# Optimization experiments

Hardware: AMD Instinct MI355X
Metric: run time of the kernel (lower is better)

Reference implementation:

```python
import jax, jax.numpy as jnp
import numpy as np

B, S, T, E, H, V = 32, 64, 64, 512, 512, 32000  # batch, src len, tgt len, embed, hidden(per dir), vocab


def _lstm_scan(xs, Wih, Whh, bih, bhh, h0, c0):
    # xs: [S, B, E]; PyTorch gate order i, f, g, o
    def step(carry, x):
        h, c = carry
        g = x @ Wih.T + bih + h @ Whh.T + bhh
        i, f, gg, o = jnp.split(g, 4, axis=-1)
        c = jax.nn.sigmoid(f) * c + jax.nn.sigmoid(i) * jnp.tanh(gg)
        h = jax.nn.sigmoid(o) * jnp.tanh(c)
        return (h, c), h
    (hT, cT), hs = jax.lax.scan(step, (h0, c0), xs)
    return hs, hT, cT


def setup_inputs() -> dict:
    key = jax.random.key(0)
    ks = jax.random.split(key, 20)
    p = lambda k, shape, s=0.05: (jax.random.normal(k, shape, jnp.float32) * s)
    inp = {
        "input_chunk": jax.random.randint(ks[0], (B, S), 0, V),
        "target_chunk": jax.random.randint(ks[1], (B, T), 0, V),
        "enc_emb": jax.random.uniform(ks[2], (V, E), jnp.float32, -0.1, 0.1),
        "dec_emb": jax.random.uniform(ks[3], (V, E), jnp.float32, -0.1, 0.1),
        # encoder bidirectional LSTM (1 layer)
        "Wih_f": p(ks[4], (4 * H, E)), "Whh_f": p(ks[5], (4 * H, H)),
        "bih_f": p(ks[6], (4 * H,)), "bhh_f": p(ks[7], (4 * H,)),
        "Wih_b": p(ks[8], (4 * H, E)), "Whh_b": p(ks[9], (4 * H, H)),
        "bih_b": p(ks[10], (4 * H,)), "bhh_b": p(ks[11], (4 * H,)),
        # decoder LSTMCell: input 2H+E, hidden 2H
        "Wih_d": p(ks[12], (8 * H, 2 * H + E)), "Whh_d": p(ks[13], (8 * H, 2 * H)),
        "bih_d": p(ks[14], (8 * H,)), "bhh_d": p(ks[15], (8 * H,)),
        # attention projection 2H -> 2H
        "Wa": p(ks[16], (2 * H, 2 * H)), "ba": p(ks[17], (2 * H,)),
        # output projection 2H -> V (bias initialized to 0 in the module)
        "Wout": p(ks[18], (V, 2 * H)), "bout": jnp.zeros((V,), jnp.float32),
    }
    return inp


def reference(input_chunk, target_chunk, enc_emb, dec_emb,
              Wih_f, Whh_f, bih_f, bhh_f, Wih_b, Whh_b, bih_b, bhh_b,
              Wih_d, Whh_d, bih_d, bhh_d, Wa, ba, Wout, bout):
    # ---- Encoder: bidirectional LSTM ----
    x = enc_emb[input_chunk]                 # [B, S, E]
    xs = jnp.transpose(x, (1, 0, 2))         # [S, B, E]
    h0 = jnp.zeros((B, H), x.dtype)
    c0 = jnp.zeros((B, H), x.dtype)
    hs_f, hT_f, cT_f = _lstm_scan(xs, Wih_f, Whh_f, bih_f, bhh_f, h0, c0)
    hs_b, hT_b, cT_b = _lstm_scan(xs[::-1], Wih_b, Whh_b, bih_b, bhh_b, h0, c0)
    hs_b = hs_b[::-1]
    all_hidden = jnp.concatenate([hs_f, hs_b], axis=-1)          # [S, B, 2H]
    all_hidden = jnp.transpose(all_hidden, (1, 0, 2))            # [B, S, 2H]
    dec_h = jnp.concatenate([hT_f, hT_b], axis=-1)               # [B, 2H]
    dec_c = jnp.concatenate([cT_f, cT_b], axis=-1)               # [B, 2H]

    # ---- Decoder: attention + LSTMCell loop (teacher forcing = 1.0, no dropout) ----
    A = all_hidden @ Wa.T + ba               # W_attention(all_hidden), constant across steps
    tgt_emb = dec_emb[target_chunk]          # [B, T, E]
    # feed at t=0 is zeros; afterwards the t-th target embedding
    feeds = jnp.concatenate([jnp.zeros((B, 1, E), tgt_emb.dtype), tgt_emb[:, :-1]], axis=1)
    feeds = jnp.transpose(feeds, (1, 0, 2))  # [T, B, E]

    def dstep(carry, feed):
        h, c = carry
        scores = jnp.einsum('bsd,bd->bs', A, h)                  # [B, S]
        attn = jax.nn.softmax(scores, axis=1)
        ctx = jnp.einsum('bs,bsd->bd', attn, all_hidden)         # [B, 2H]
        inp = jnp.concatenate([ctx, feed], axis=1)               # [B, 2H+E]
        g = inp @ Wih_d.T + bih_d + h @ Whh_d.T + bhh_d
        i, f, gg, o = jnp.split(g, 4, axis=-1)
        c = jax.nn.sigmoid(f) * c + jax.nn.sigmoid(i) * jnp.tanh(gg)
        h = jax.nn.sigmoid(o) * jnp.tanh(c)
        logits = h @ Wout.T + bout                               # [B, V]
        return (h, c), logits

    _, logits = jax.lax.scan(dstep, (dec_h, dec_c), feeds)       # [T, B, V]
    logits = jnp.transpose(logits, (1, 0, 2))                    # [B, T, V]
    outputs = jnp.argmax(logits, axis=-1)                        # [B, T]
    return logits, outputs
```

## Files before the change

kernel.cpp:

```cpp
#include <hip/hip_runtime.h>
#include <hip/hip_bf16.h>

#define BB 32
#define SS 64
#define TT 64
#define EE 512
#define HH 512
#define VV 32000

#define O_C0    0u
#define O_C1    32768u
#define O_HD    65536u
#define O_CD    98304u
#define O_PENC  131072u
#define O_PDEC  655360u
#define O_CTX   1179648u
#define O_ALLH  1212416u
#define O_AATT  3309568u
#define O_HDEC  5406720u
#define O_PACK  7503872u
#define O_DA1   7507968u
#define O_DA2   7540736u
#define O_W1    7573504u
#define WS_NEED 95830016ull

#define S_GXF   0u
#define S_GXB   4194304u
#define S_GFEED 8388608u
#define U_BASE  17000000u
#define U_WIHF  10485760u
#define U_WIHB  11534336u
#define U_WFEED 12582912u
#define U_TOTAL 14680064u

typedef float f32x4 __attribute__((ext_vector_type(4)));
typedef _Float16 f16x8 __attribute__((ext_vector_type(8)));
typedef _Float16 f16x4 __attribute__((ext_vector_type(4)));

__device__ __forceinline__ float sigm_(float x){ return 1.0f/(1.0f + expf(-x)); }

__device__ __forceinline__ unsigned int fkey_(float f){
  unsigned int u = __float_as_uint(f);
  return (u & 0x80000000u) ? ~u : (u | 0x80000000u);
}

__device__ __forceinline__ int swz_(int row, int kb){
  return (row*64 + kb) ^ ((row & 7) << 4);
}

__global__ __launch_bounds__(256) void k_init(float* __restrict__ ws){
  int i = blockIdx.x*256 + threadIdx.x;
  if (i < 65536) ws[i] = 0.0f;
  if (i < 2048) ((unsigned long long*)(ws + O_PACK))[i] = 0ull;
}

__global__ __launch_bounds__(256) void k_cvtW(
    const float* __restrict__ Whh_f, const float* __restrict__ Whh_b,
    const float* __restrict__ Wih_d, const float* __restrict__ Whh_d,
    const float* __restrict__ Wih_f, const float* __restrict__ Wih_b,
    _Float16* __restrict__ dst)
{
  int g = blockIdx.x*256 + threadIdx.x;
  unsigned idx = (unsigned)g*4u;
  if (idx >= U_TOTAL) return;
  f32x4 v;
  if (idx < 1048576u){
    v = *(const f32x4*)(Whh_f + idx);
  } else if (idx < 2097152u){
    v = *(const f32x4*)(Whh_b + (idx - 1048576u));
  } else if (idx < U_WIHF){
    unsigned j = idx - 2097152u;
    unsigned row = j >> 11, col = j & 2047u;
    const float* src = (col < 1024u) ? (Wih_d + (size_t)row*1536 + col)
                                     : (Whh_d + (size_t)row*1024 + (col - 1024u));
    v = *(const f32x4*)src;
  } else if (idx < U_WIHB){
    v = *(const f32x4*)(Wih_f + (idx - U_WIHF));
  } else if (idx < U_WFEED){
    v = *(const f32x4*)(Wih_b + (idx - U_WIHB));
  } else {
    unsigned j = idx - U_WFEED;
    unsigned row = j >> 9, col = j & 511u;
    v = *(const f32x4*)(Wih_d + (size_t)row*1536 + 1024 + col);
  }
  f16x4 h;
  #pragma unroll
  for (int c = 0; c < 4; ++c) h[c] = (_Float16)v[c];
  *(f16x4*)(dst + idx) = h;
}

__global__ __launch_bounds__(256) void k_cvtWout(
    const float* __restrict__ Wout, _Float16* __restrict__ W1)
{
  size_t i = ((size_t)blockIdx.x*256 + threadIdx.x)*8;
  f32x4 x0 = *(const f32x4*)(Wout + i);
  f32x4 x1 = *(const f32x4*)(Wout + i + 4);
  f16x4 h0, h1;
  #pragma unroll
  for (int c = 0; c < 4; ++c){ h0[c] = (_Float16)x0[c]; h1[c] = (_Float16)x1[c]; }
  *(f16x4*)(W1 + i)   = h0;
  *(f16x4*)(W1 + i+4) = h1;
}

template<int MODE>
__global__ __launch_bounds__(256) void k_gemm(
    const float* __restrict__ A, int lda,
    const int* __restrict__ chunk,
    const float* __restrict__ W, int ldW,
    const float* __restrict__ bias0, const float* __restrict__ bias1,
    float* __restrict__ C, int ldC, int K)
{
  __shared__ float As[16*68];
  __shared__ float Bs[16*68];
  int tid = threadIdx.x;
  int n0 = blockIdx.x*64, m0 = blockIdx.y*64;
  int tx = tid & 15, ty = tid >> 4;
  int lrow = tid >> 2, kq = tid & 3;

  const float* arp;
  if (MODE == 0) {
    arp = A + (size_t)(m0 + lrow)*lda;
  } else if (MODE == 1) {
    int m = m0 + lrow; int s = m >> 5, b = m & 31;
    arp = A + (size_t)chunk[b*SS + s]*EE;
  } else {
    int m = m0 + lrow; int t = m >> 5, b = m & 31;
    arp = (t == 0) ? nullptr : A + (size_t)chunk[b*TT + (t-1)]*EE;
  }
  const float* wrp = W + (size_t)(n0 + lrow)*ldW;

  float acc[4][4] = {};
  for (int k0 = 0; k0 < K; k0 += 16){
    float4 va = make_float4(0.f,0.f,0.f,0.f);
    if (MODE == 0) va = *(const float4*)&arp[k0 + kq*4];
    else if (arp)  va = *(const float4*)&arp[k0 + kq*4];
    float4 vw = *(const float4*)&wrp[k0 + kq*4];
    As[(kq*4+0)*68 + lrow] = va.x;
    As[(kq*4+1)*68 + lrow] = va.y;
    As[(kq*4+2)*68 + lrow] = va.z;
    As[(kq*4+3)*68 + lrow] = va.w;
    Bs[(kq*4+0)*68 + lrow] = vw.x;
    Bs[(kq*4+1)*68 + lrow] = vw.y;
    Bs[(kq*4+2)*68 + lrow] = vw.z;
    Bs[(kq*4+3)*68 + lrow] = vw.w;
    __syncthreads();
    #pragma unroll
    for (int kk = 0; kk < 16; ++kk){
      float4 a4 = *(const float4*)&As[kk*68 + ty*4];
      float4 b4 = *(const float4*)&Bs[kk*68 + tx*4];
      float av[4] = {a4.x,a4.y,a4.z,a4.w};
      float bv[4] = {b4.x,b4.y,b4.z,b4.w};
      #pragma unroll
      for (int i=0;i<4;++i)
        #pragma unroll
        for (int j=0;j<4;++j)
          acc[i][j] = fmaf(av[i], bv[j], acc[i][j]);
    }
    __syncthreads();
  }
  float bv[4];
  #pragma unroll
  for (int j = 0; j < 4; ++j){
    int n = n0 + tx*4 + j;
    float bb = 0.f;
    if (bias0) bb += bias0[n];
    if (bias1) bb += bias1[n];
    bv[j] = bb;
  }
  #pragma unroll
  for (int i = 0; i < 4; ++i){
    int m = m0 + ty*4 + i;
    float4 v = make_float4(acc[i][0]+bv[0], acc[i][1]+bv[1], acc[i][2]+bv[2], acc[i][3]+bv[3]);
    *(float4*)&C[(size_t)m*ldC + n0 + tx*4] = v;
  }
}

template<int MODE>
__global__ __launch_bounds__(256) void k_proj(
    const float* __restrict__ emb, const int* __restrict__ chunk,
    const _Float16* __restrict__ Wh,
    const float* __restrict__ bias0, const float* __restrict__ bias1,
    float* __restrict__ C, int ldC)
{
  __shared__ char lds[49152];
  int tid = threadIdx.x;
  int n0 = blockIdx.x*128, m0 = blockIdx.y*128;
  int lane = tid & 63, wave = tid >> 6;
  int wm = wave >> 1, wn = wave & 1;
  int lr = lane & 15, lg = lane >> 4;

  int s0 = tid*2, s1 = tid*2 + 1;
  int ar0 = s0 >> 2, as0 = s0 & 3;
  int ar1 = s1 >> 2, as1 = s1 & 3;

  const float* arp0; const float* arp1;
  {
    int m = m0 + ar0;
    if (MODE == 1){ int s = m >> 5, b = m & 31; arp0 = emb + (size_t)chunk[b*SS + s]*EE + as0*8; }
    else { int tt = m >> 5, b = m & 31; arp0 = tt ? (emb + (size_t)chunk[b*TT + (tt-1)]*EE + as0*8) : nullptr; }
    m = m0 + ar1;
    if (MODE == 1){ int s = m >> 5, b = m & 31; arp1 = emb + (size_t)chunk[b*SS + s]*EE + as1*8; }
    else { int tt = m >> 5, b = m & 31; arp1 = tt ? (emb + (size_t)chunk[b*TT + (tt-1)]*EE + as1*8) : nullptr; }
  }
  const _Float16* wp0 = Wh + (size_t)(n0 + ar0)*512u + as0*8;
  const _Float16* wp1 = Wh + (size_t)(n0 + ar1)*512u + as1*8;

  f32x4 accH[4][4], accM[4][4];
  #pragma unroll
  for (int i = 0; i < 4; ++i)
    #pragma unroll
    for (int j = 0; j < 4; ++j){
      f32x4 z; z[0]=z[1]=z[2]=z[3]=0.f;
      accH[i][j] = z; accM[i][j] = z;
    }

  f32x4 zz; zz[0]=zz[1]=zz[2]=zz[3]=0.f;
  f32x4 a0a, a0b, a1a, a1b;
  uint4 rw0, rw1;
  a0a = arp0 ? *(const f32x4*)(arp0)     : zz;
  a0b = arp0 ? *(const f32x4*)(arp0 + 4) : zz;
  a1a = arp1 ? *(const f32x4*)(arp1)     : zz;
  a1b = arp1 ? *(const f32x4*)(arp1 + 4) : zz;
  rw0 = *(const uint4*)wp0;
  rw1 = *(const uint4*)wp1;

  for (int kt = 0; kt < 16; ++kt){
    char* base = lds + (kt & 1)*24576;
    char* A1t = base, *A2t = base + 8192, *Wt = base + 16384;
    f16x8 h0, l0, h1, l1;
    #pragma unroll
    for (int c = 0; c < 4; ++c){
      float x = a0a[c]; _Float16 hh = (_Float16)x;
      h0[c] = hh; l0[c] = (_Float16)((x - (float)hh)*2048.0f);
      x = a0b[c]; hh = (_Float16)x;
      h0[4+c] = hh; l0[4+c] = (_Float16)((x - (float)hh)*2048.0f);
      x = a1a[c]; hh = (_Float16)x;
      h1[c] = hh; l1[c] = (_Float16)((x - (float)hh)*2048.0f);
      x = a1b[c]; hh = (_Float16)x;
      h1[4+c] = hh; l1[4+c] = (_Float16)((x - (float)hh)*2048.0f);
    }
    *(f16x8*)(A1t + swz_(ar0, as0*16)) = h0;
    *(f16x8*)(A2t + swz_(ar0, as0*16)) = l0;
    *(f16x8*)(A1t + swz_(ar1, as1*16)) = h1;
    *(f16x8*)(A2t + swz_(ar1, as1*16)) = l1;
    *(uint4*)(Wt + swz_(ar0, as0*16)) = rw0;
    *(uint4*)(Wt + swz_(ar1, as1*16)) = rw1;
    __syncthreads();
    if (kt < 15){
      int ko = (kt+1)*32;
      a0a = arp0 ? *(const f32x4*)(arp0 + ko)     : zz;
      a0b = arp0 ? *(const f32x4*)(arp0 + ko + 4) : zz;
      a1a = arp1 ? *(const f32x4*)(arp1 + ko)     : zz;
      a1b = arp1 ? *(const f32x4*)(arp1 + ko + 4) : zz;
      rw0 = *(const uint4*)(wp0 + ko);
      rw1 = *(const uint4*)(wp1 + ko);
    }
    f16x8 wf[4];
    #pragma unroll
    for (int nf = 0; nf < 4; ++nf)
      wf[nf] = *(const f16x8*)(Wt + swz_(wn*64 + nf*16 + lr, lg*16));
    #pragma unroll
    for (int mf = 0; mf < 4; ++mf){
      int ad = swz_(wm*64 + mf*16 + lr, lg*16);
      f16x8 a1f = *(const f16x8*)(A1t + ad);
      f16x8 a2f = *(const f16x8*)(A2t + ad);
      #pragma unroll
      for (int nf = 0; nf < 4; ++nf){
        accH[mf][nf] = __builtin_amdgcn_mfma_f32_16x16x32_f16(a1f, wf[nf], accH[mf][nf], 0, 0, 0);
        accM[mf][nf] = __builtin_amdgcn_mfma_f32_16x16x32_f16(a2f, wf[nf], accM[mf][nf], 0, 0, 0);
      }
    }
    __syncthreads();
  }

  const float rs = 1.0f/2048.0f;
  float bb[4];
  #pragma unroll
  for (int nf = 0; nf < 4; ++nf){
    int n = n0 + wn*64 + nf*16 + lr;
    bb[nf] = bias0[n] + bias1[n];
  }
  #pragma unroll
  for (int mf = 0; mf < 4; ++mf){
    #pragma unroll
    for (int r = 0; r < 4; ++r){
      int m = m0 + wm*64 + mf*16 + lg*4 + r;
      #pragma unroll
      for (int nf = 0; nf < 4; ++nf){
        int n = n0 + wn*64 + nf*16 + lr;
        C[(size_t)m*ldC + n] = accH[mf][nf][r] + accM[mf][nf][r]*rs + bb[nf];
      }
    }
  }
}

__global__ __launch_bounds__(256) void k_enc_step(
    const _Float16* __restrict__ wenc,
    float* __restrict__ ws, const float* __restrict__ oscr, int t)
{
  __shared__ float hl[128*36];
  __shared__ float Wt[32*132];
  int sub = blockIdx.x, kp = blockIdx.y, dir = blockIdx.z;
  int tid = threadIdx.x;
  int s = dir ? (63 - t) : t;
  int p = t & 1;
  const float* gx  = oscr + (dir ? S_GXB : S_GXF);
  const float* prd = ws + (p ? O_PDEC : O_PENC) + dir*262144u;
  const float* cin = ws + O_C0 + p*32768u + dir*16384u;
  float* cout = ws + O_C0 + (p^1)*32768u + dir*16384u;

  {
    int ug = tid & 31, bg = tid >> 5;
    int ul0 = ug*4;
    int u0 = kp*128 + ul0;
    #pragma unroll
    for (int j = 0; j < 4; ++j){
      int b = bg*4 + j;
      size_t gbase = (size_t)(s*32 + b)*2048u;
      f32x4 g0 = *(const f32x4*)&gx[gbase + u0];
      f32x4 g1 = *(const f32x4*)&gx[gbase + 512 + u0];
      f32x4 g2 = *(const f32x4*)&gx[gbase + 1024 + u0];
      f32x4 g3 = *(const f32x4*)&gx[gbase + 1536 + u0];
      if (t > 0){
        #pragma unroll
        for (int kq = 0; kq < 4; ++kq){
          const float* pp = prd + kq*65536u + (size_t)b*2048u;
          g0 += *(const f32x4*)&pp[u0];
          g1 += *(const f32x4*)&pp[512 + u0];
          g2 += *(const f32x4*)&pp[1024 + u0];
          g3 += *(const f32x4*)&pp[1536 + u0];
        }
      }
      f32x4 c = *(const f32x4*)&cin[b*512 + u0];
      f32x4 cn, hn;
      #pragma unroll
      for (int e = 0; e < 4; ++e){
        float cc = sigm_(g1[e])*c[e] + sigm_(g0[e])*tanhf(g2[e]);
        float hh = sigm_(g3[e])*tanhf(cc);
        cn[e] = cc; hn[e] = hh;
        hl[(ul0+e)*36 + b] = hh;
      }
      if (sub == 0){
        *(f32x4*)&cout[b*512 + u0] = cn;
        *(f32x4*)&ws[O_ALLH + (size_t)(b*64 + s)*1024u + dir*512 + u0] = hn;
      }
    }
  }
  __syncthreads();
  if (t == 63) return;

  const _Float16* W = wenc + dir*1048576u;
  float* P = ws + (p ? O_PENC : O_PDEC) + dir*262144u + kp*65536u;
  int rg2 = tid & 31, bg2 = tid >> 5;
  int wrow = tid & 127, whalf = tid >> 7;
  float acc[4][4] = {};
  for (int kt = 0; kt < 4; ++kt){
    #pragma unroll
    for (int i = 0; i < 4; ++i){
      int chunk = whalf*4 + i;
      int grow = sub*128 + wrow;
      f16x4 v = *(const f16x4*)&W[(size_t)grow*512 + kp*128 + kt*32 + chunk*4];
      Wt[(chunk*4+0)*132 + wrow] = (float)v[0];
      Wt[(chunk*4+1)*132 + wrow] = (float)v[1];
      Wt[(chunk*4+2)*132 + wrow] = (float)v[2];
      Wt[(chunk*4+3)*132 + wrow] = (float)v[3];
    }
    __syncthreads();
    #pragma unroll 8
    for (int kk = 0; kk < 32; ++kk){
      f32x4 wv = *(const f32x4*)&Wt[kk*132 + rg2*4];
      f32x4 hv = *(const f32x4*)&hl[(kt*32+kk)*36 + bg2*4];
      #pragma unroll
      for (int i = 0; i < 4; ++i)
        #pragma unroll
        for (int j = 0; j < 4; ++j)
          acc[i][j] = fmaf(wv[i], hv[j], acc[i][j]);
    }
    __syncthreads();
  }
  #pragma unroll
  for (int j = 0; j < 4; ++j){
    int b = bg2*4 + j;
    f32x4 v; v[0]=acc[0][j]; v[1]=acc[1][j]; v[2]=acc[2][j]; v[3]=acc[3][j];
    *(f32x4*)&P[(size_t)b*2048u + sub*128 + rg2*4] = v;
  }
}

__global__ __launch_bounds__(256) void k_concat(float* __restrict__ ws){
  int i = blockIdx.x*256 + threadIdx.x;
  int which = i >> 15;
  int idx = i & 32767;
  int b = idx >> 10, u = idx & 1023;
  int dir = (u >= 512);
  int uu = u & 511;
  float v;
  if (which == 0){
    int s = dir ? 0 : 63;
    v = ws[O_ALLH + (size_t)(b*64 + s)*1024u + u];
  } else {
    v = ws[O_C0 + dir*16384u + b*512 + uu];
  }
  ws[(which ? O_CD : O_HD) + b*1024 + u] = v;
}

__global__ __launch_bounds__(256) void k_dec_gemm(
    const _Float16* __restrict__ wdec, float* __restrict__ ws)
{
  __shared__ char lds[16384];
  int nb = blockIdx.x, kp = blockIdx.y;
  int tid = threadIdx.x;
  int lane = tid & 63, w = tid >> 6;
  int lr = lane & 15, lg = lane >> 4;
  const _Float16* A1g = (const _Float16*)(ws + O_DA1);
  const _Float16* A2g = (const _Float16*)(ws + O_DA2);

  int aslot = tid & 127;
  int isA2  = tid >> 7;
  int arow = aslot >> 2, aseg = aslot & 3;
  int wrow = tid >> 2, wseg = tid & 3;
  const _Float16* asrc = (isA2 ? A2g : A1g) + (size_t)arow*2048u + kp*512 + aseg*8;
  const _Float16* wsrc = wdec + (size_t)(nb*64 + wrow)*2048u + kp*512 + wseg*8;

  f32x4 accH[2], accM[2];
  #pragma unroll
  for (int i = 0; i < 2; ++i){ f32x4 z; z[0]=z[1]=z[2]=z[3]=0.f; accH[i]=z; accM[i]=z; }

  uint4 rA = *(const uint4*)(asrc);
  uint4 rW = *(const uint4*)(wsrc);

  for (int kt = 0; kt < 16; ++kt){
    int cur = kt & 1;
    char* base = lds + cur*8192;
    *(uint4*)(base + (isA2 ? 2048 : 0) + swz_(arow, aseg*16)) = rA;
    *(uint4*)(base + 4096 + swz_(wrow, wseg*16)) = rW;
    __syncthreads();
    if (kt < 15){
      rA = *(const uint4*)(asrc + (kt+1)*32);
      rW = *(const uint4*)(wsrc + (kt+1)*32);
    }
    char* A1t = base, *A2t = base + 2048, *Wt = base + 4096;
    f16x8 wf = *(const f16x8*)(Wt + swz_(w*16 + lr, lg*16));
    #pragma unroll
    for (int mf = 0; mf < 2; ++mf){
      f16x8 a1 = *(const f16x8*)(A1t + swz_(mf*16 + lr, lg*16));
      f16x8 a2 = *(const f16x8*)(A2t + swz_(mf*16 + lr, lg*16));
      accH[mf] = __builtin_amdgcn_mfma_f32_16x16x32_f16(a1, wf, accH[mf], 0, 0, 0);
      accM[mf] = __builtin_amdgcn_mfma_f32_16x16x32_f16(a2, wf, accM[mf], 0, 0, 0);
    }
    __syncthreads();
  }
  const float rs = 1.0f/2048.0f;
  float* P = ws + O_PDEC + (size_t)kp*131072u;
  #pragma unroll
  for (int mf = 0; mf < 2; ++mf)
    #pragma unroll
    for (int r = 0; r < 4; ++r){
      int b = mf*16 + lg*4 + r;
      int n = nb*64 + w*16 + lr;
      P[(size_t)b*4096u + n] = accH[mf][r] + accM[mf][r]*rs;
    }
}

__global__ __launch_bounds__(256) void k_attn(float* __restrict__ ws,
                                              const float* __restrict__ oscr, int t){
  __shared__ float hlq[1024];
  __shared__ float part[64][5];
  __shared__ float sc[64];
  __shared__ float atn[64];
  __shared__ float dsh;
  int b = blockIdx.x, tid = threadIdx.x;
  float* hd = ws + O_HD;
  float* cd = ws + O_CD;
  _Float16* DA1 = (_Float16*)(ws + O_DA1);
  _Float16* DA2 = (_Float16*)(ws + O_DA2);
  if (t > 0){
    const float* gfd = oscr + S_GFEED + (size_t)((t-1)*32 + b)*4096u;
    const float* pd = ws + O_PDEC;
    for (int u = tid; u < 1024; u += 256){
      float g0 = gfd[u], g1 = gfd[1024+u], g2 = gfd[2048+u], g3 = gfd[3072+u];
      #pragma unroll
      for (int kp = 0; kp < 4; ++kp){
        const float* p = pd + (size_t)kp*131072u + (size_t)b*4096u;
        g0 += p[u]; g1 += p[1024+u]; g2 += p[2048+u]; g3 += p[3072+u];
      }
      float c = cd[b*1024 + u];
      c = sigm_(g1)*c + sigm_(g0)*tanhf(g2);
      float h = sigm_(g3)*tanhf(c);
      cd[b*1024+u] = c; hd[b*1024+u] = h; hlq[u] = h;
      ws[O_HDEC + (size_t)(b*64 + (t-1))*1024u + u] = h;
      _Float16 hi = (_Float16)h;
      DA1[(size_t)b*2048u + 1024 + u] = hi;
      DA2[(size_t)b*2048u + 1024 + u] = (_Float16)((h - (float)hi)*2048.0f);
    }
  } else {
    for (int u = tid; u < 1024; u += 256){
      float h = hd[b*1024 + u];
      hlq[u] = h;
      _Float16 hi = (_Float16)h;
      DA1[(size_t)b*2048u + 1024 + u] = hi;
      DA2[(size_t)b*2048u + 1024 + u] = (_Float16)((h - (float)hi)*2048.0f);
    }
  }
  __syncthreads();
  {
    int s = tid >> 2, p = tid & 3;
    const float* Ar = ws + O_AATT + (size_t)(b*64 + s)*1024u + p*256;
    const float* hp = &hlq[p*256];
    float sum = 0.f;
    #pragma unroll 8
    for (int k4 = 0; k4 < 64; ++k4){
      float4 a = *(const float4*)&Ar[k4*4];
      float4 h4 = *(const float4*)&hp[k4*4];
      sum = fmaf(a.x,h4.x, fmaf(a.y,h4.y, fmaf(a.z,h4.z, fmaf(a.w,h4.w, sum))));
    }
    part[s][p] = sum;
  }
  __syncthreads();
  if (tid < 64) sc[tid] = part[tid][0] + part[tid][1] + part[tid][2] + part[tid][3];
  __syncthreads();
  if (tid < 64){
    float m = sc[0];
    #pragma unroll
    for (int i = 1; i < 64; ++i) m = fmaxf(m, sc[i]);
    atn[tid] = expf(sc[tid] - m);
  }
  __syncthreads();
  if (tid == 0){
    float d = 0.f;
    #pragma unroll
    for (int i = 0; i < 64; ++i) d += atn[i];
    dsh = 1.0f/d;
  }
  __syncthreads();
  {
    float rd = dsh;
    float ax=0.f, ay=0.f, az=0.f, aw=0.f;
    const float* ah = ws + O_ALLH + (size_t)(b*64)*1024u + tid*4;
    for (int s2 = 0; s2 < 64; ++s2){
      float a = atn[s2];
      float4 v = *(const float4*)&ah[(size_t)s2*1024u];
      ax = fmaf(a, v.x, ax); ay = fmaf(a, v.y, ay);
      az = fmaf(a, v.z, az); aw = fmaf(a, v.w, aw);
    }
    float o[4] = {ax*rd, ay*rd, az*rd, aw*rd};
    #pragma unroll
    for (int j = 0; j < 4; ++j){
      int u = tid*4 + j;
      _Float16 hi = (_Float16)o[j];
      DA1[(size_t)b*2048u + u] = hi;
      DA2[(size_t)b*2048u + u] = (_Float16)((o[j] - (float)hi)*2048.0f);
    }
  }
}

__global__ __launch_bounds__(256) void k_fin(float* __restrict__ ws,
                                             const float* __restrict__ oscr){
  int bid = blockIdx.x, tid = threadIdx.x;
  if ((bid & 3) == 3){
    int b = bid >> 2;
    const float* gfd = oscr + S_GFEED + (size_t)(63*32 + b)*4096u;
    const float* pd = ws + O_PDEC;
    for (int q = 0; q < 4; ++q){
      int u = q*256 + tid;
      float g0 = gfd[u], g1 = gfd[1024+u], g2 = gfd[2048+u], g3 = gfd[3072+u];
      #pragma unroll
      for (int kp = 0; kp < 4; ++kp){
        const float* p = pd + (size_t)kp*131072u + (size_t)b*4096u;
        g0 += p[u]; g1 += p[1024+u]; g2 += p[2048+u]; g3 += p[3072+u];
      }
      float c = ws[O_CD + b*1024 + u];
      c = sigm_(g1)*c + sigm_(g0)*tanhf(g2);
      float h = sigm_(g3)*tanhf(c);
      ws[O_HDEC + (size_t)(b*64 + 63)*1024u + u] = h;
    }
  }
  __syncthreads();
  const float* src = ws + O_HDEC;
  _Float16* A1 = (_Float16*)(ws + O_ALLH);
  _Float16* A2 = (_Float16*)(ws + O_AATT);
  for (int rep = 0; rep < 8; ++rep){
    int i = bid*16384 + (rep*256 + tid)*8;
    f32x4 x0 = *(const f32x4*)&src[i];
    f32x4 x1 = *(const f32x4*)&src[i+4];
    f16x4 h0, h1, l0, l1;
    #pragma unroll
    for (int c = 0; c < 4; ++c){
      _Float16 a = (_Float16)x0[c];
      h0[c] = a; l0[c] = (_Float16)((x0[c] - (float)a)*2048.0f);
      _Float16 bq = (_Float16)x1[c];
      h1[c] = bq; l1[c] = (_Float16)((x1[c] - (float)bq)*2048.0f);
    }
    *(f16x4*)&A1[i]   = h0;
    *(f16x4*)&A1[i+4] = h1;
    *(f16x4*)&A2[i]   = l0;
    *(f16x4*)&A2[i+4] = l1;
  }
}

__global__ __launch_bounds__(256) void k_logits(
    const _Float16* __restrict__ A1, const _Float16* __restrict__ A2,
    const _Float16* __restrict__ W1, const float* __restrict__ bout,
    float* __restrict__ out, unsigned long long* __restrict__ pk)
{
  __shared__ char lds[49152];
  int tid = threadIdx.x;
  int n0 = blockIdx.y*128, m0 = blockIdx.x*128;
  int lane = tid & 63, wave = tid >> 6;
  int wm = wave >> 1, wn = wave & 1;
  int lr = lane & 15, lg = lane >> 4;

  int s0 = tid*2, s1 = tid*2 + 1;
  int ar0 = s0 >> 2, as0 = s0 & 3;
  int ar1 = s1 >> 2, as1 = s1 & 3;
  const _Float16* a1p0 = A1 + (size_t)(m0 + ar0)*1024u + as0*8;
  const _Float16* a1p1 = A1 + (size_t)(m0 + ar1)*1024u + as1*8;
  const _Float16* a2p0 = A2 + (size_t)(m0 + ar0)*1024u + as0*8;
  const _Float16* a2p1 = A2 + (size_t)(m0 + ar1)*1024u + as1*8;
  const _Float16* wp0  = W1 + (size_t)(n0 + ar0)*1024u + as0*8;
  const _Float16* wp1  = W1 + (size_t)(n0 + ar1)*1024u + as1*8;

  f32x4 accH[4][4], accM[4][4];
  #pragma unroll
  for (int i = 0; i < 4; ++i)
    #pragma unroll
    for (int j = 0; j < 4; ++j){
      f32x4 z; z[0]=z[1]=z[2]=z[3]=0.f;
      accH[i][j] = z; accM[i][j] = z;
    }

  uint4 r10, r11, r20, r21, rw0, rw1;
  r10 = *(const uint4*)a1p0; r11 = *(const uint4*)a1p1;
  r20 = *(const uint4*)a2p0; r21 = *(const uint4*)a2p1;
  rw0 = *(const uint4*)wp0;  rw1 = *(const uint4*)wp1;

  for (int kt = 0; kt < 32; ++kt){
    int cur = kt & 1;
    char* base = lds + cur*24576;
    char* A1t = base, *A2t = base + 8192, *Wt = base + 16384;
    *(uint4*)(A1t + swz_(ar0, as0*16)) = r10;
    *(uint4*)(A1t + swz_(ar1, as1*16)) = r11;
    *(uint4*)(A2t + swz_(ar0, as0*16)) = r20;
    *(uint4*)(A2t + swz_(ar1, as1*16)) = r21;
    *(uint4*)(Wt  + swz_(ar0, as0*16)) = rw0;
    *(uint4*)(Wt  + swz_(ar1, as1*16)) = rw1;
    __syncthreads();
    if (kt < 31){
      int ko = (kt+1)*32;
      r10 = *(const uint4*)(a1p0 + ko); r11 = *(const uint4*)(a1p1 + ko);
      r20 = *(const uint4*)(a2p0 + ko); r21 = *(const uint4*)(a2p1 + ko);
      rw0 = *(const uint4*)(wp0 + ko);  rw1 = *(const uint4*)(wp1 + ko);
    }
    f16x8 wf[4];
    #pragma unroll
    for (int nf = 0; nf < 4; ++nf)
      wf[nf] = *(const f16x8*)(Wt + swz_(wn*64 + nf*16 + lr, lg*16));
    #pragma unroll
    for (int mf = 0; mf < 4; ++mf){
      int ad = swz_(wm*64 + mf*16 + lr, lg*16);
      f16x8 a1f = *(const f16x8*)(A1t + ad);
      f16x8 a2f = *(const f16x8*)(A2t + ad);
      #pragma unroll
      for (int nf = 0; nf < 4; ++nf){
        accH[mf][nf] = __builtin_amdgcn_mfma_f32_16x16x32_f16(a1f, wf[nf], accH[mf][nf], 0, 0, 0);
        accM[mf][nf] = __builtin_amdgcn_mfma_f32_16x16x32_f16(a2f, wf[nf], accM[mf][nf], 0, 0, 0);
      }
    }
    __syncthreads();
  }

  const float rs = 1.0f/2048.0f;
  float bb[4];
  #pragma unroll
  for (int nf = 0; nf < 4; ++nf) bb[nf] = bout[n0 + wn*64 + nf*16 + lr];
  #pragma unroll
  for (int mf = 0; mf < 4; ++mf){
    #pragma unroll
    for (int r = 0; r < 4; ++r){
      int m = m0 + wm*64 + mf*16 + lg*4 + r;
      unsigned long long bk = 0ull;
      #pragma unroll
      for (int nf = 0; nf < 4; ++nf){
        int n = n0 + wn*64 + nf*16 + lr;
        float val = accH[mf][nf][r] + accM[mf][nf][r]*rs + bb[nf];
        __builtin_nontemporal_store(val, &out[(size_t)m*VV + n]);
        unsigned long long p = ((unsigned long long)fkey_(val) << 32) | (unsigned int)(~(unsigned int)n);
        if (p > bk) bk = p;
      }
      #pragma unroll
      for (int off = 1; off < 16; off <<= 1){
        unsigned long long o = __shfl_xor(bk, off, 64);
        if (o > bk) bk = o;
      }
      if (lr == 0) atomicMax(&pk[m], bk);
    }
  }
}

__global__ __launch_bounds__(512) void k_logits_fb(
    const _Float16* __restrict__ A1, const _Float16* __restrict__ A2,
    const float* __restrict__ Wout, const float* __restrict__ bout,
    float* __restrict__ out, unsigned long long* __restrict__ pk)
{
  __shared__ char lds[49152];
  char* A1t = lds;
  char* A2t = lds + 8192;
  char* W1t = lds + 16384;
  char* W2t = lds + 32768;
  int tid = threadIdx.x;
  int n0 = blockIdx.x*256;
  int lane = tid & 63, wave = tid >> 6;
  int wm = wave >> 2, wn = wave & 3;
  int lr = lane & 15, lg = lane >> 4;

  int arow = tid >> 2, aseg = tid & 3;
  int wrow = tid >> 1, wseg = tid & 1;
  const float* wp = Wout + (size_t)(n0 + wrow)*1024u + wseg*16;

  float bb[4];
  #pragma unroll
  for (int nf = 0; nf < 4; ++nf) bb[nf] = bout[n0 + wn*64 + nf*16 + lr];
  const float rs = 1.0f/2048.0f;

  for (int mi = 0; mi < 4; ++mi){
    int m0 = (blockIdx.y*4 + mi)*128;
    const _Float16* a1p = A1 + (size_t)(m0 + arow)*1024u + aseg*8;
    const _Float16* a2p = A2 + (size_t)(m0 + arow)*1024u + aseg*8;

    f32x4 accH[4][4], accM[4][4];
    #pragma unroll
    for (int i = 0; i < 4; ++i)
      #pragma unroll
      for (int j = 0; j < 4; ++j){
        f32x4 z; z[0]=z[1]=z[2]=z[3]=0.f;
        accH[i][j] = z; accM[i][j] = z;
      }

    for (int k0 = 0; k0 < 1024; k0 += 32){
      uint4 av1 = *(const uint4*)(a1p + k0);
      uint4 av2 = *(const uint4*)(a2p + k0);
      f32x4 wv[4];
      #pragma unroll
      for (int i = 0; i < 4; ++i) wv[i] = *(const f32x4*)(wp + k0 + i*4);
      __syncthreads();
      *(uint4*)(A1t + swz_(arow, aseg*16)) = av1;
      *(uint4*)(A2t + swz_(arow, aseg*16)) = av2;
      f16x8 hi[2], lo[2];
      #pragma unroll
      for (int i = 0; i < 2; ++i)
        #pragma unroll
        for (int c = 0; c < 8; ++c){
          float x = wv[i*2 + (c>>2)][c&3];
          _Float16 h = (_Float16)x;
          hi[i][c] = h;
          lo[i][c] = (_Float16)((x - (float)h)*2048.0f);
        }
      *(f16x8*)(W1t + swz_(wrow, wseg*32 +  0)) = hi[0];
      *(f16x8*)(W1t + swz_(wrow, wseg*32 + 16)) = hi[1];
      *(f16x8*)(W2t + swz_(wrow, wseg*32 +  0)) = lo[0];
      *(f16x8*)(W2t + swz_(wrow, wseg*32 + 16)) = lo[1];
      __syncthreads();
      f16x8 w1f[4], w2f[4];
      #pragma unroll
      for (int nf = 0; nf < 4; ++nf){
        int ad = swz_(wn*64 + nf*16 + lr, lg*16);
        w1f[nf] = *(const f16x8*)(W1t + ad);
        w2f[nf] = *(const f16x8*)(W2t + ad);
      }
      #pragma unroll
      for (int mf = 0; mf < 4; ++mf){
        int ad = swz_(wm*64 + mf*16 + lr, lg*16);
        f16x8 a1f = *(const f16x8*)(A1t + ad);
        f16x8 a2f = *(const f16x8*)(A2t + ad);
        #pragma unroll
        for (int nf = 0; nf < 4; ++nf){
          accH[mf][nf] = __builtin_amdgcn_mfma_f32_16x16x32_f16(a1f, w1f[nf], accH[mf][nf], 0, 0, 0);
          accM[mf][nf] = __builtin_amdgcn_mfma_f32_16x16x32_f16(a1f, w2f[nf], accM[mf][nf], 0, 0, 0);
          accM[mf][nf] = __builtin_amdgcn_mfma_f32_16x16x32_f16(a2f, w1f[nf], accM[mf][nf], 0, 0, 0);
        }
      }
    }

    #pragma unroll
    for (int mf = 0; mf < 4; ++mf){
      #pragma unroll
      for (int r = 0; r < 4; ++r){
        int m = m0 + wm*64 + mf*16 + lg*4 + r;
        unsigned long long bk = 0ull;
        #pragma unroll
        for (int nf = 0; nf < 4; ++nf){
          int n = n0 + wn*64 + nf*16 + lr;
          float val = accH[mf][nf][r] + accM[mf][nf][r]*rs + bb[nf];
          __builtin_nontemporal_store(val, &out[(size_t)m*VV + n]);
          unsigned long long p = ((unsigned long long)fkey_(val) << 32) | (unsigned int)(~(unsigned int)n);
          if (p > bk) bk = p;
        }
        #pragma unroll
        for (int off = 1; off < 16; off <<= 1){
          unsigned long long o = __shfl_xor(bk, off, 64);
          if (o > bk) bk = o;
        }
        if (lr == 0) atomicMax(&pk[m], bk);
      }
    }
  }
}

__global__ __launch_bounds__(256) void k_argmax(
    const unsigned long long* __restrict__ pk, float* __restrict__ out)
{
  int i = blockIdx.x*256 + threadIdx.x;
  if (i < 2048){
    unsigned int low = (unsigned int)(pk[i] & 0xFFFFFFFFull);
    unsigned int col = ~low;
    out[(size_t)BB*TT*VV + i] = (float)col;
  }
}

extern "C" void kernel_launch(void* const* d_in, const int* in_sizes, int n_in,
                              void* d_out, int out_size, void* d_ws, size_t ws_size,
                              hipStream_t stream)
{
  const int*   input_chunk  = (const int*)d_in[0];
  const int*   target_chunk = (const int*)d_in[1];
  const float* enc_emb = (const float*)d_in[2];
  const float* dec_emb = (const float*)d_in[3];
  const float* Wih_f = (const float*)d_in[4];
  const float* Whh_f = (const float*)d_in[5];
  const float* bih_f = (const float*)d_in[6];
  const float* bhh_f = (const float*)d_in[7];
  const float* Wih_b = (const float*)d_in[8];
  const float* Whh_b = (const float*)d_in[9];
  const float* bih_b = (const float*)d_in[10];
  const float* bhh_b = (const float*)d_in[11];
  const float* Wih_d = (const float*)d_in[12];
  const float* Whh_d = (const float*)d_in[13];
  const float* bih_d = (const float*)d_in[14];
  const float* bhh_d = (const float*)d_in[15];
  const float* Wa   = (const float*)d_in[16];
  const float* ba   = (const float*)d_in[17];
  const float* Wout = (const float*)d_in[18];
  const float* bout = (const float*)d_in[19];
  float* ws = (float*)d_ws;
  float* out = (float*)d_out;
  float* oscr = (float*)d_out;
  _Float16* wf16 = (_Float16*)(oscr + U_BASE);
  bool bigws = (ws_size >= WS_NEED);

  k_init<<<256, 256, 0, stream>>>(ws);
  k_cvtW<<<14336, 256, 0, stream>>>(Whh_f, Whh_b, Wih_d, Whh_d, Wih_f, Wih_b, wf16);
  if (bigws)
    k_cvtWout<<<16000, 256, 0, stream>>>(Wout, (_Float16*)(ws + O_W1));

  k_proj<1><<<dim3(16,16), 256, 0, stream>>>(enc_emb, input_chunk, wf16 + U_WIHF, bih_f, bhh_f, oscr + S_GXF, 2048);
  k_proj<1><<<dim3(16,16), 256, 0, stream>>>(enc_emb, input_chunk, wf16 + U_WIHB, bih_b, bhh_b, oscr + S_GXB, 2048);
  k_proj<2><<<dim3(32,16), 256, 0, stream>>>(dec_emb, target_chunk, wf16 + U_WFEED, bih_d, bhh_d, oscr + S_GFEED, 4096);

  for (int t = 0; t < 64; ++t){
    k_enc_step<<<dim3(16,4,2), 256, 0, stream>>>(wf16, ws, oscr, t);
  }

  k_concat<<<256, 256, 0, stream>>>(ws);
  k_gemm<0><<<dim3(16,32), 256, 0, stream>>>(ws + O_ALLH, 1024, nullptr, Wa, 1024, ba, nullptr, ws + O_AATT, 1024, 1024);

  const _Float16* wdec = wf16 + 2097152u;
  for (int t = 0; t < 64; ++t){
    k_attn<<<32, 256, 0, stream>>>(ws, oscr, t);
    k_dec_gemm<<<dim3(64,4), 256, 0, stream>>>(wdec, ws);
  }
  k_fin<<<128, 256, 0, stream>>>(ws, oscr);

  if (bigws){
    k_logits<<<dim3(16,250), 256, 0, stream>>>(
        (const _Float16*)(ws + O_ALLH), (const _Float16*)(ws + O_AATT),
        (const _Float16*)(ws + O_W1), bout, out, (unsigned long long*)(ws + O_PACK));
  } else {
    k_logits_fb<<<dim3(125,4), 512, 0, stream>>>(
        (const _Float16*)(ws + O_ALLH), (const _Float16*)(ws + O_AATT),
        Wout, bout, out, (unsigned long long*)(ws + O_PACK));
  }
  k_argmax<<<8, 256, 0, stream>>>((const unsigned long long*)(ws + O_PACK), out);
}
```

Measured before the change: 3.315 ms.

## Route attention projection through MFMA proj kernel and stream logits A-operand from registers

Replaces the scalar FP32 tiled GEMM for the attention projection (all_hidden @ Wa) with the existing split-fp16 MFMA projection kernel, generalized to a runtime K and a plain row-major mode. Wa is converted to fp16 along with the other weights. Separately, the logits kernel now loads the A1/A2 fragments directly from global memory into registers, prefetched one k-step ahead, and stages only the weight tile in LDS. This cuts LDS use and traffic, at the cost of uncoalesced per-lane global loads and more live registers.

```diff
diff --git a/kernel.cpp b/kernel.cpp
--- a/kernel.cpp
+++ b/kernel.cpp
@@ -10,11 +10,10 @@
 
 #define O_C0    0u
 #define O_C1    32768u
+#define O_PENC  131072u
+#define O_PDEC  655360u
 #define O_HD    65536u
 #define O_CD    98304u
-#define O_PENC  131072u
-#define O_PDEC  655360u
-#define O_CTX   1179648u
 #define O_ALLH  1212416u
 #define O_AATT  3309568u
 #define O_HDEC  5406720u
@@ -31,7 +30,8 @@
 #define U_WIHF  10485760u
 #define U_WIHB  11534336u
 #define U_WFEED 12582912u
-#define U_TOTAL 14680064u
+#define U_WA    14680064u
+#define U_TOTAL 15728640u
 
 typedef float f32x4 __attribute__((ext_vector_type(4)));
 typedef _Float16 f16x8 __attribute__((ext_vector_type(8)));
@@ -58,6 +58,7 @@
     const float* __restrict__ Whh_f, const float* __restrict__ Whh_b,
     const float* __restrict__ Wih_d, const float* __restrict__ Whh_d,
     const float* __restrict__ Wih_f, const float* __restrict__ Wih_b,
+    const float* __restrict__ Wa,
     _Float16* __restrict__ dst)
 {
   int g = blockIdx.x*256 + threadIdx.x;
@@ -78,10 +79,12 @@
     v = *(const f32x4*)(Wih_f + (idx - U_WIHF));
   } else if (idx < U_WFEED){
     v = *(const f32x4*)(Wih_b + (idx - U_WIHB));
-  } else {
+  } else if (idx < U_WA){
     unsigned j = idx - U_WFEED;
     unsigned row = j >> 9, col = j & 511u;
     v = *(const f32x4*)(Wih_d + (size_t)row*1536 + 1024 + col);
+  } else {
+    v = *(const f32x4*)(Wa + (idx - U_WA));
   }
   f16x4 h;
   #pragma unroll
@@ -103,81 +106,8 @@
 }
 
 template<int MODE>
-__global__ __launch_bounds__(256) void k_gemm(
-    const float* __restrict__ A, int lda,
-    const int* __restrict__ chunk,
-    const float* __restrict__ W, int ldW,
-    const float* __restrict__ bias0, const float* __restrict__ bias1,
-    float* __restrict__ C, int ldC, int K)
-{
-  __shared__ float As[16*68];
-  __shared__ float Bs[16*68];
-  int tid = threadIdx.x;
-  int n0 = blockIdx.x*64, m0 = blockIdx.y*64;
-  int tx = tid & 15, ty = tid >> 4;
-  int lrow = tid >> 2, kq = tid & 3;
-
-  const float* arp;
-  if (MODE == 0) {
-    arp = A + (size_t)(m0 + lrow)*lda;
-  } else if (MODE == 1) {
-    int m = m0 + lrow; int s = m >> 5, b = m & 31;
-    arp = A + (size_t)chunk[b*SS + s]*EE;
-  } else {
-    int m = m0 + lrow; int t = m >> 5, b = m & 31;
-    arp = (t == 0) ? nullptr : A + (size_t)chunk[b*TT + (t-1)]*EE;
-  }
-  const float* wrp = W + (size_t)(n0 + lrow)*ldW;
-
-  float acc[4][4] = {};
-  for (int k0 = 0; k0 < K; k0 += 16){
-    float4 va = make_float4(0.f,0.f,0.f,0.f);
-    if (MODE == 0) va = *(const float4*)&arp[k0 + kq*4];
-    else if (arp)  va = *(const float4*)&arp[k0 + kq*4];
-    float4 vw = *(const float4*)&wrp[k0 + kq*4];
-    As[(kq*4+0)*68 + lrow] = va.x;
-    As[(kq*4+1)*68 + lrow] = va.y;
-    As[(kq*4+2)*68 + lrow] = va.z;
-    As[(kq*4+3)*68 + lrow] = va.w;
-    Bs[(kq*4+0)*68 + lrow] = vw.x;
-    Bs[(kq*4+1)*68 + lrow] = vw.y;
-    Bs[(kq*4+2)*68 + lrow] = vw.z;
-    Bs[(kq*4+3)*68 + lrow] = vw.w;
-    __syncthreads();
-    #pragma unroll
-    for (int kk = 0; kk < 16; ++kk){
-      float4 a4 = *(const float4*)&As[kk*68 + ty*4];
-      float4 b4 = *(const float4*)&Bs[kk*68 + tx*4];
-      float av[4] = {a4.x,a4.y,a4.z,a4.w};
-      float bv[4] = {b4.x,b4.y,b4.z,b4.w};
-      #pragma unroll
-      for (int i=0;i<4;++i)
-        #pragma unroll
-        for (int j=0;j<4;++j)
-          acc[i][j] = fmaf(av[i], bv[j], acc[i][j]);
-    }
-    __syncthreads();
-  }
-  float bv[4];
-  #pragma unroll
-  for (int j = 0; j < 4; ++j){
-    int n = n0 + tx*4 + j;
-    float bb = 0.f;
-    if (bias0) bb += bias0[n];
-    if (bias1) bb += bias1[n];
-    bv[j] = bb;
-  }
-  #pragma unroll
-  for (int i = 0; i < 4; ++i){
-    int m = m0 + ty*4 + i;
-    float4 v = make_float4(acc[i][0]+bv[0], acc[i][1]+bv[1], acc[i][2]+bv[2], acc[i][3]+bv[3]);
-    *(float4*)&C[(size_t)m*ldC + n0 + tx*4] = v;
-  }
-}
-
-template<int MODE>
 __global__ __launch_bounds__(256) void k_proj(
-    const float* __restrict__ emb, const int* __restrict__ chunk,
+    const float* __restrict__ Asrc, const int* __restrict__ chunk, int K,
     const _Float16* __restrict__ Wh,
     const float* __restrict__ bias0, const float* __restrict__ bias1,
     float* __restrict__ C, int ldC)
@@ -196,14 +126,16 @@
   const float* arp0; const float* arp1;
   {
     int m = m0 + ar0;
-    if (MODE == 1){ int s = m >> 5, b = m & 31; arp0 = emb + (size_t)chunk[b*SS + s]*EE + as0*8; }
-    else { int tt = m >> 5, b = m & 31; arp0 = tt ? (emb + (size_t)chunk[b*TT + (tt-1)]*EE + as0*8) : nullptr; }
+    if (MODE == 0){ arp0 = Asrc + (size_t)m*K + as0*8; }
+    else if (MODE == 1){ int s = m >> 5, b = m & 31; arp0 = Asrc + (size_t)chunk[b*SS + s]*EE + as0*8; }
+    else { int tt = m >> 5, b = m & 31; arp0 = tt ? (Asrc + (size_t)chunk[b*TT + (tt-1)]*EE + as0*8) : nullptr; }
     m = m0 + ar1;
-    if (MODE == 1){ int s = m >> 5, b = m & 31; arp1 = emb + (size_t)chunk[b*SS + s]*EE + as1*8; }
-    else { int tt = m >> 5, b = m & 31; arp1 = tt ? (emb + (size_t)chunk[b*TT + (tt-1)]*EE + as1*8) : nullptr; }
-  }
-  const _Float16* wp0 = Wh + (size_t)(n0 + ar0)*512u + as0*8;
-  const _Float16* wp1 = Wh + (size_t)(n0 + ar1)*512u + as1*8;
+    if (MODE == 0){ arp1 = Asrc + (size_t)m*K + as1*8; }
+    else if (MODE == 1){ int s = m >> 5, b = m & 31; arp1 = Asrc + (size_t)chunk[b*SS + s]*EE + as1*8; }
+    else { int tt = m >> 5, b = m & 31; arp1 = tt ? (Asrc + (size_t)chunk[b*TT + (tt-1)]*EE + as1*8) : nullptr; }
+  }
+  const _Float16* wp0 = Wh + (size_t)(n0 + ar0)*K + as0*8;
+  const _Float16* wp1 = Wh + (size_t)(n0 + ar1)*K + as1*8;
 
   f32x4 accH[4][4], accM[4][4];
   #pragma unroll
@@ -224,7 +156,8 @@
   rw0 = *(const uint4*)wp0;
   rw1 = *(const uint4*)wp1;
 
-  for (int kt = 0; kt < 16; ++kt){
+  int kiters = K >> 5;
+  for (int kt = 0; kt < kiters; ++kt){
     char* base = lds + (kt & 1)*24576;
     char* A1t = base, *A2t = base + 8192, *Wt = base + 16384;
     f16x8 h0, l0, h1, l1;
@@ -246,7 +179,7 @@
     *(uint4*)(Wt + swz_(ar0, as0*16)) = rw0;
     *(uint4*)(Wt + swz_(ar1, as1*16)) = rw1;
     __syncthreads();
-    if (kt < 15){
+    if (kt < kiters-1){
       int ko = (kt+1)*32;
       a0a = arp0 ? *(const f32x4*)(arp0 + ko)     : zz;
       a0b = arp0 ? *(const f32x4*)(arp0 + ko + 4) : zz;
@@ -278,7 +211,7 @@
   #pragma unroll
   for (int nf = 0; nf < 4; ++nf){
     int n = n0 + wn*64 + nf*16 + lr;
-    bb[nf] = bias0[n] + bias1[n];
+    bb[nf] = bias0[n] + (bias1 ? bias1[n] : 0.0f);
   }
   #pragma unroll
   for (int mf = 0; mf < 4; ++mf){
@@ -602,7 +535,7 @@
     const _Float16* __restrict__ W1, const float* __restrict__ bout,
     float* __restrict__ out, unsigned long long* __restrict__ pk)
 {
-  __shared__ char lds[49152];
+  __shared__ char lds[16384];
   int tid = threadIdx.x;
   int n0 = blockIdx.y*128, m0 = blockIdx.x*128;
   int lane = tid & 63, wave = tid >> 6;
@@ -610,14 +543,13 @@
   int lr = lane & 15, lg = lane >> 4;
 
   int s0 = tid*2, s1 = tid*2 + 1;
-  int ar0 = s0 >> 2, as0 = s0 & 3;
-  int ar1 = s1 >> 2, as1 = s1 & 3;
-  const _Float16* a1p0 = A1 + (size_t)(m0 + ar0)*1024u + as0*8;
-  const _Float16* a1p1 = A1 + (size_t)(m0 + ar1)*1024u + as1*8;
-  const _Float16* a2p0 = A2 + (size_t)(m0 + ar0)*1024u + as0*8;
-  const _Float16* a2p1 = A2 + (size_t)(m0 + ar1)*1024u + as1*8;
-  const _Float16* wp0  = W1 + (size_t)(n0 + ar0)*1024u + as0*8;
-  const _Float16* wp1  = W1 + (size_t)(n0 + ar1)*1024u + as1*8;
+  int wr0 = s0 >> 2, wg0 = s0 & 3;
+  int wr1 = s1 >> 2, wg1 = s1 & 3;
+  const _Float16* wp0 = W1 + (size_t)(n0 + wr0)*1024u + wg0*8;
+  const _Float16* wp1 = W1 + (size_t)(n0 + wr1)*1024u + wg1*8;
+
+  const _Float16* a1b = A1 + (size_t)(m0 + wm*64 + lr)*1024u + lg*8;
+  const _Float16* a2b = A2 + (size_t)(m0 + wm*64 + lr)*1024u + lg*8;
 
   f32x4 accH[4][4], accM[4][4];
   #pragma unroll
@@ -628,43 +560,47 @@
       accH[i][j] = z; accM[i][j] = z;
     }
 
-  uint4 r10, r11, r20, r21, rw0, rw1;
-  r10 = *(const uint4*)a1p0; r11 = *(const uint4*)a1p1;
-  r20 = *(const uint4*)a2p0; r21 = *(const uint4*)a2p1;
-  rw0 = *(const uint4*)wp0;  rw1 = *(const uint4*)wp1;
+  uint4 rw0 = *(const uint4*)wp0;
+  uint4 rw1 = *(const uint4*)wp1;
+  f16x8 a1f[4], a2f[4];
+  #pragma unroll
+  for (int mf = 0; mf < 4; ++mf){
+    a1f[mf] = *(const f16x8*)(a1b + mf*16*1024);
+    a2f[mf] = *(const f16x8*)(a2b + mf*16*1024);
+  }
 
   for (int kt = 0; kt < 32; ++kt){
-    int cur = kt & 1;
-    char* base = lds + cur*24576;
-    char* A1t = base, *A2t = base + 8192, *Wt = base + 16384;
-    *(uint4*)(A1t + swz_(ar0, as0*16)) = r10;
-    *(uint4*)(A1t + swz_(ar1, as1*16)) = r11;
-    *(uint4*)(A2t + swz_(ar0, as0*16)) = r20;
-    *(uint4*)(A2t + swz_(ar1, as1*16)) = r21;
-    *(uint4*)(Wt  + swz_(ar0, as0*16)) = rw0;
-    *(uint4*)(Wt  + swz_(ar1, as1*16)) = rw1;
+    char* Wt = lds + (kt & 1)*8192;
+    *(uint4*)(Wt + swz_(wr0, wg0*16)) = rw0;
+    *(uint4*)(Wt + swz_(wr1, wg1*16)) = rw1;
     __syncthreads();
     if (kt < 31){
       int ko = (kt+1)*32;
-      r10 = *(const uint4*)(a1p0 + ko); r11 = *(const uint4*)(a1p1 + ko);
-      r20 = *(const uint4*)(a2p0 + ko); r21 = *(const uint4*)(a2p1 + ko);
-      rw0 = *(const uint4*)(wp0 + ko);  rw1 = *(const uint4*)(wp1 + ko);
+      rw0 = *(const uint4*)(wp0 + ko);
+      rw1 = *(const uint4*)(wp1 + ko);
     }
     f16x8 wf[4];
     #pragma unroll
     for (int nf = 0; nf < 4; ++nf)
       wf[nf] = *(const f16x8*)(Wt + swz_(wn*64 + nf*16 + lr, lg*16));
-    #pragma unroll
-    for (int mf = 0; mf < 4; ++mf){
-      int ad = swz_(wm*64 + mf*16 + lr, lg*16);
-      f16x8 a1f = *(const f16x8*)(A1t + ad);
-      f16x8 a2f = *(const f16x8*)(A2t + ad);
+    f16x8 c1[4], c2[4];
+    #pragma unroll
+    for (int mf = 0; mf < 4; ++mf){ c1[mf] = a1f[mf]; c2[mf] = a2f[mf]; }
+    if (kt < 31){
+      int ko = (kt+1)*32;
+      #pragma unroll
+      for (int mf = 0; mf < 4; ++mf){
+        a1f[mf] = *(const f16x8*)(a1b + mf*16*1024 + ko);
+        a2f[mf] = *(const f16x8*)(a2b + mf*16*1024 + ko);
+      }
+    }
+    #pragma unroll
+    for (int mf = 0; mf < 4; ++mf)
       #pragma unroll
       for (int nf = 0; nf < 4; ++nf){
-        accH[mf][nf] = __builtin_amdgcn_mfma_f32_16x16x32_f16(a1f, wf[nf], accH[mf][nf], 0, 0, 0);
-        accM[mf][nf] = __builtin_amdgcn_mfma_f32_16x16x32_f16(a2f, wf[nf], accM[mf][nf], 0, 0, 0);
-      }
-    }
+        accH[mf][nf] = __builtin_amdgcn_mfma_f32_16x16x32_f16(c1[mf], wf[nf], accH[mf][nf], 0, 0, 0);
+        accM[mf][nf] = __builtin_amdgcn_mfma_f32_16x16x32_f16(c2[mf], wf[nf], accM[mf][nf], 0, 0, 0);
+      }
     __syncthreads();
   }
 
@@ -847,20 +783,20 @@
   bool bigws = (ws_size >= WS_NEED);
 
   k_init<<<256, 256, 0, stream>>>(ws);
-  k_cvtW<<<14336, 256, 0, stream>>>(Whh_f, Whh_b, Wih_d, Whh_d, Wih_f, Wih_b, wf16);
+  k_cvtW<<<15360, 256, 0, stream>>>(Whh_f, Whh_b, Wih_d, Whh_d, Wih_f, Wih_b, Wa, wf16);
   if (bigws)
     k_cvtWout<<<16000, 256, 0, stream>>>(Wout, (_Float16*)(ws + O_W1));
 
-  k_proj<1><<<dim3(16,16), 256, 0, stream>>>(enc_emb, input_chunk, wf16 + U_WIHF, bih_f, bhh_f, oscr + S_GXF, 2048);
-  k_proj<1><<<dim3(16,16), 256, 0, stream>>>(enc_emb, input_chunk, wf16 + U_WIHB, bih_b, bhh_b, oscr + S_GXB, 2048);
-  k_proj<2><<<dim3(32,16), 256, 0, stream>>>(dec_emb, target_chunk, wf16 + U_WFEED, bih_d, bhh_d, oscr + S_GFEED, 4096);
+  k_proj<1><<<dim3(16,16), 256, 0, stream>>>(enc_emb, input_chunk, 512, wf16 + U_WIHF, bih_f, bhh_f, oscr + S_GXF, 2048);
+  k_proj<1><<<dim3(16,16), 256, 0, stream>>>(enc_emb, input_chunk, 512, wf16 + U_WIHB, bih_b, bhh_b, oscr + S_GXB, 2048);
+  k_proj<2><<<dim3(32,16), 256, 0, stream>>>(dec_emb, target_chunk, 512, wf16 + U_WFEED, bih_d, bhh_d, oscr + S_GFEED, 4096);
 
   for (int t = 0; t < 64; ++t){
     k_enc_step<<<dim3(16,4,2), 256, 0, stream>>>(wf16, ws, oscr, t);
   }
 
   k_concat<<<256, 256, 0, stream>>>(ws);
-  k_gemm<0><<<dim3(16,32), 256, 0, stream>>>(ws + O_ALLH, 1024, nullptr, Wa, 1024, ba, nullptr, ws + O_AATT, 1024, 1024);
+  k_proj<0><<<dim3(8,16), 256, 0, stream>>>(ws + O_ALLH, nullptr, 1024, wf16 + U_WA, ba, nullptr, ws + O_AATT, 1024);
 
   const _Float16* wdec = wf16 + 2097152u;
   for (int t = 0; t < 64; ++t){
```

Measured after the change: 3.726 ms. 12.4% more time.
